# Kernel optimization log

Measured on AMD Instinct MI355X. Metric: run time of the kernel, lower is better.

Reference implementation:

```python
import math
import jax, jax.numpy as jnp
import numpy as np

B, H, S, D = 2, 16, 2048, 1024
DK = D // H  # 64


def setup_inputs() -> dict:
    key = jax.random.key(0)
    k1, k2, k3, k4, k5 = jax.random.split(key, 5)
    scale = np.float32(0.02)
    return {
        "x": jax.random.normal(k1, (B, H, S, D), dtype=jnp.float32),
        "wq": jax.random.normal(k2, (DK, D), dtype=jnp.float32) * scale,
        "wk": jax.random.normal(k3, (DK, D), dtype=jnp.float32) * scale,
        "wv": jax.random.normal(k4, (DK, D), dtype=jnp.float32) * scale,
        "wo": jax.random.normal(k5, (D, D), dtype=jnp.float32) * scale,
    }


def reference(x, wq, wk, wv, wo):
    # x: [B, H, S, D]; wq/wk/wv: [dk, D]; wo: [D, D]
    b, h, s, d = x.shape
    xq = jnp.einsum("bhsd,kd->bhsk", x, wq)  # [B,H,S,dk]
    xk = jnp.einsum("bhsd,kd->bhsk", x, wk)
    xv = jnp.einsum("bhsd,kd->bhsk", x, wv)
    # NOTE: original scales by sqrt(hidden_dim), not sqrt(dk)
    inv_scale = np.float32(1.0 / math.sqrt(d))
    score = jnp.einsum("bhsk,bhtk->bhst", xq, xk) * inv_scale  # [B,H,S,S]
    attn = jax.nn.softmax(score, axis=-1).astype(xq.dtype)
    out = jnp.einsum("bhst,bhtk->bhsk", attn, xv)  # [B,H,S,dk]
    out = out.transpose(0, 2, 1, 3).reshape(b, s, h * (wq.shape[0]))  # [B,S,H*dk]
    return out @ wo.T  # [B,S,D]
```

## Files before the change

### kernel.cpp

```cpp
#include <hip/hip_runtime.h>
#include <math.h>

#define BB 2
#define HH 16
#define SS 2048
#define DD 1024
#define DK 64
#define BHS (BB*HH*SS)
#define QSCALE 0.04508422f

typedef short  bf16x8  __attribute__((ext_vector_type(8)));
typedef float  floatx4 __attribute__((ext_vector_type(4)));
typedef unsigned short u16;

#define MFMA(a,b,c) __builtin_amdgcn_mfma_f32_16x16x32_bf16((a),(b),(c),0,0,0)

__device__ __forceinline__ unsigned cvt_pk_bf16(float lo, float hi) {
    unsigned r;
    asm("v_cvt_pk_bf16_f32 %0, %1, %2" : "=v"(r) : "v"(lo), "v"(hi));
    return r;
}
__device__ __forceinline__ bf16x8 ldfrag(const u16* p) {
    union { uint4 u; bf16x8 b; } c;
    c.u = *(const uint4*)p;
    return c.b;
}
__device__ __forceinline__ void stbf4(u16* p, float4 t) {
    union { unsigned u[2]; uint2 v; } c;
    c.u[0] = cvt_pk_bf16(t.x, t.y);
    c.u[1] = cvt_pk_bf16(t.z, t.w);
    *(uint2*)p = c.v;
}
__device__ __forceinline__ void st4s(u16* p, float a, float b, float c, float d) {
    unsigned x = cvt_pk_bf16(a, b), y = cvt_pk_bf16(c, d);
    p[0]  = (u16)x; p[16] = (u16)(x >> 16);
    p[32] = (u16)y; p[48] = (u16)(y >> 16);
}
__device__ __forceinline__ void st2s(u16* p, float a, float b) {
    unsigned x = cvt_pk_bf16(a, b);
    p[0]  = (u16)x; p[16] = (u16)(x >> 16);
}

#define WQKV_CHUNKS (192*1024/4)
#define WO_CHUNKS   (1024*1024/4)
__global__ __launch_bounds__(256) void convert_w(
    const float* __restrict__ wq, const float* __restrict__ wk,
    const float* __restrict__ wv, const float* __restrict__ wo,
    u16* __restrict__ wqkv, u16* __restrict__ wo_bf)
{
    int i = blockIdx.x * 256 + threadIdx.x;
    if (i < WQKV_CHUNKS) {
        int r = i >> 8;
        int c = i & 255;
        const float* src = (r < 64) ? wq : ((r < 128) ? wk : wv);
        float4 t = *(const float4*)(src + (size_t)(r & 63) * DD + c * 4);
        stbf4(wqkv + (size_t)r * DD + c * 4, t);
    } else if (i < WQKV_CHUNKS + WO_CHUNKS) {
        int j = i - WQKV_CHUNKS;
        float4 t = *(const float4*)(wo + (size_t)j * 4);
        stbf4(wo_bf + (size_t)j * 4, t);
    }
}

__global__ __launch_bounds__(512) void qkv_proj(
    const float* __restrict__ x, const u16* __restrict__ wqkv,
    u16* __restrict__ q, u16* __restrict__ k, u16* __restrict__ vT)
{
    __shared__ __align__(16) u16 Ws[2][192][72];
    const int tid  = threadIdx.x;
    const int w    = tid >> 6;
    const int lane = tid & 63;
    const int quad = lane >> 4;
    const int l16  = lane & 15;
    const int rt   = w & 3;
    const int g    = w >> 2;
    const int rowbase = blockIdx.x * 64;
    const float* xr = x + (size_t)(rowbase + rt * 16 + l16) * DD + quad * 8;

    uint4 wreg[3];
    auto wload = [&](int kk) {
#pragma unroll
        for (int it = 0; it < 3; ++it) {
            int li = tid + it * 512;
            int r  = li >> 3, c8 = li & 7;
            wreg[it] = *(const uint4*)(wqkv + (size_t)r * DD + kk * 64 + c8 * 8);
        }
    };
    auto wstore = [&](int p) {
#pragma unroll
        for (int it = 0; it < 3; ++it) {
            int li = tid + it * 512;
            int r  = li >> 3, c8 = li & 7;
            *(uint4*)&Ws[p][r][c8 * 8] = wreg[it];
        }
    };

    float4 xc[4], xn[4];
    auto xload = [&](int kk, float4* d) {
        const float* p = xr + kk * 64;
        d[0] = *(const float4*)(p);
        d[1] = *(const float4*)(p + 4);
        d[2] = *(const float4*)(p + 32);
        d[3] = *(const float4*)(p + 36);
    };

    floatx4 acc[6];
#pragma unroll
    for (int j = 0; j < 6; ++j) acc[j] = (floatx4){0.f,0.f,0.f,0.f};

    wload(0); wstore(0);
    xload(0, xc);
    __syncthreads();

    for (int kk = 0; kk < 16; ++kk) {
        int p = kk & 1;
        if (kk < 15) { wload(kk + 1); xload(kk + 1, xn); }
        union { unsigned u[4]; bf16x8 v; } A0, A1;
        A0.u[0] = cvt_pk_bf16(xc[0].x, xc[0].y);
        A0.u[1] = cvt_pk_bf16(xc[0].z, xc[0].w);
        A0.u[2] = cvt_pk_bf16(xc[1].x, xc[1].y);
        A0.u[3] = cvt_pk_bf16(xc[1].z, xc[1].w);
        A1.u[0] = cvt_pk_bf16(xc[2].x, xc[2].y);
        A1.u[1] = cvt_pk_bf16(xc[2].z, xc[2].w);
        A1.u[2] = cvt_pk_bf16(xc[3].x, xc[3].y);
        A1.u[3] = cvt_pk_bf16(xc[3].z, xc[3].w);
#pragma unroll
        for (int j = 0; j < 6; ++j) {
            int n = g * 6 + j;
            bf16x8 b0 = ldfrag(&Ws[p][n * 16 + l16][quad * 8]);
            bf16x8 b1 = ldfrag(&Ws[p][n * 16 + l16][32 + quad * 8]);
            acc[j] = MFMA(A0.v, b0, acc[j]);
            acc[j] = MFMA(A1.v, b1, acc[j]);
        }
        if (kk < 15) {
            wstore(p ^ 1);
#pragma unroll
            for (int i2 = 0; i2 < 4; ++i2) xc[i2] = xn[i2];
            __syncthreads();
        }
    }

    u16 (*Vbuf)[72] = (u16 (*)[72])&Ws[0][0][0];
#pragma unroll
    for (int rr = 0; rr < 4; ++rr) {
        int rloc = rt * 16 + quad * 4 + rr;
        size_t m = (size_t)(rowbase + rloc);
        if (g == 0) {
            st4s(&q[m * DK + l16], acc[0][rr] * QSCALE, acc[1][rr] * QSCALE,
                                   acc[2][rr] * QSCALE, acc[3][rr] * QSCALE);
            st2s(&k[m * DK + l16], acc[4][rr], acc[5][rr]);
        } else {
            st2s(&k[m * DK + 32 + l16], acc[0][rr], acc[1][rr]);
            st4s(&Vbuf[rloc][l16], acc[2][rr], acc[3][rr],
                                   acc[4][rr], acc[5][rr]);
        }
    }
    __syncthreads();
    {
        const int dk = tid >> 3;
        const int sc = (tid & 7) * 8;
        const int bh = rowbase >> 11;
        const int s0 = rowbase & 2047;
        union { u16 s[8]; uint4 u; } t;
#pragma unroll
        for (int u = 0; u < 8; ++u) t.s[u] = Vbuf[sc + u][dk];
        *(uint4*)(vT + ((size_t)(bh * DK + dk)) * SS + s0 + sc) = t.u;
    }
}

__global__ __launch_bounds__(256) void flash_attn(
    const u16* __restrict__ q, const u16* __restrict__ k,
    const u16* __restrict__ vT, u16* __restrict__ ao)
{
    __shared__ __align__(16) u16 Qs[64][72];
    __shared__ __align__(16) u16 Ks[64][72];
    __shared__ __align__(16) u16 Vt[64][72];
    __shared__ __align__(16) u16 Ps[4][16][72];
    const int tid  = threadIdx.x;
    const int w    = tid >> 6;
    const int lane = tid & 63;
    const int quad = lane >> 4;
    const int l16  = lane & 15;
    const int qt   = blockIdx.x;
    const int bh   = blockIdx.y;
    const size_t kbase = (size_t)bh * SS * DK;
    const size_t vbase = (size_t)bh * DK * SS;

#pragma unroll
    for (int it = 0; it < 2; ++it) {
        int li = tid + it * 256;
        int r  = li >> 3, c8 = li & 7;
        *(uint4*)&Qs[r][c8 * 8] =
            *(const uint4*)(q + kbase + (size_t)(qt * 64 + r) * DK + c8 * 8);
    }

    float m_i[4], l_i[4];
    floatx4 acc_o[4];
#pragma unroll
    for (int r = 0; r < 4; ++r) { m_i[r] = -INFINITY; l_i[r] = 0.f; }
#pragma unroll
    for (int n = 0; n < 4; ++n) acc_o[n] = (floatx4){0.f,0.f,0.f,0.f};
    __syncthreads();

    for (int kt = 0; kt < SS / 64; ++kt) {
#pragma unroll
        for (int it = 0; it < 2; ++it) {
            int li = tid + it * 256;
            int r  = li >> 3, c8 = li & 7;
            *(uint4*)&Ks[r][c8 * 8] =
                *(const uint4*)(k + kbase + (size_t)(kt * 64 + r) * DK + c8 * 8);
            *(uint4*)&Vt[r][c8 * 8] =
                *(const uint4*)(vT + vbase + (size_t)r * SS + kt * 64 + c8 * 8);
        }
        __syncthreads();

        floatx4 sc[4];
        __builtin_amdgcn_s_setprio(1);
        {
            bf16x8 a0 = ldfrag(&Qs[w * 16 + l16][quad * 8]);
            bf16x8 a1 = ldfrag(&Qs[w * 16 + l16][32 + quad * 8]);
#pragma unroll
            for (int n = 0; n < 4; ++n) {
                sc[n] = (floatx4){0.f,0.f,0.f,0.f};
                bf16x8 b0 = ldfrag(&Ks[n * 16 + l16][quad * 8]);
                bf16x8 b1 = ldfrag(&Ks[n * 16 + l16][32 + quad * 8]);
                sc[n] = MFMA(a0, b0, sc[n]);
                sc[n] = MFMA(a1, b1, sc[n]);
            }
        }
        __builtin_amdgcn_s_setprio(0);

        float rmx[4];
#pragma unroll
        for (int r = 0; r < 4; ++r) {
            float rm = fmaxf(fmaxf(sc[0][r], sc[1][r]), fmaxf(sc[2][r], sc[3][r]));
#pragma unroll
            for (int off = 1; off < 16; off <<= 1)
                rm = fmaxf(rm, __shfl_xor(rm, off, 64));
            rmx[r] = rm;
        }
        int ok = (rmx[0] <= m_i[0] + 8.f) & (rmx[1] <= m_i[1] + 8.f) &
                 (rmx[2] <= m_i[2] + 8.f) & (rmx[3] <= m_i[3] + 8.f);
        if (!__all(ok)) {
#pragma unroll
            for (int r = 0; r < 4; ++r) {
                float mnew  = fmaxf(m_i[r], rmx[r]);
                float alpha = __builtin_amdgcn_exp2f(m_i[r] - mnew);
#pragma unroll
                for (int n = 0; n < 4; ++n) acc_o[n][r] *= alpha;
                l_i[r] *= alpha;
                m_i[r]  = mnew;
            }
        }
#pragma unroll
        for (int r = 0; r < 4; ++r) {
            float mi = m_i[r];
            float p0 = __builtin_amdgcn_exp2f(sc[0][r] - mi);
            float p1 = __builtin_amdgcn_exp2f(sc[1][r] - mi);
            float p2 = __builtin_amdgcn_exp2f(sc[2][r] - mi);
            float p3 = __builtin_amdgcn_exp2f(sc[3][r] - mi);
            float rs = (p0 + p1) + (p2 + p3);
#pragma unroll
            for (int off = 1; off < 16; off <<= 1)
                rs += __shfl_xor(rs, off, 64);
            l_i[r] += rs;
            st4s(&Ps[w][quad * 4 + r][l16], p0, p1, p2, p3);
        }

        __builtin_amdgcn_s_setprio(1);
#pragma unroll
        for (int kc = 0; kc < 2; ++kc) {
            bf16x8 a = ldfrag(&Ps[w][l16][kc * 32 + quad * 8]);
#pragma unroll
            for (int n = 0; n < 4; ++n) {
                bf16x8 b = ldfrag(&Vt[n * 16 + l16][kc * 32 + quad * 8]);
                acc_o[n] = MFMA(a, b, acc_o[n]);
            }
        }
        __builtin_amdgcn_s_setprio(0);
        __syncthreads();
    }

    const int b = bh >> 4, h = bh & 15;
#pragma unroll
    for (int r = 0; r < 4; ++r) {
        int srow = qt * 64 + w * 16 + quad * 4 + r;
        float rl = __builtin_amdgcn_rcpf(l_i[r]);
        size_t base = ((size_t)(b * SS + srow)) * (HH * DK) + h * 64;
        st4s(&ao[base + l16], acc_o[0][r] * rl, acc_o[1][r] * rl,
                              acc_o[2][r] * rl, acc_o[3][r] * rl);
    }
}

__global__ __launch_bounds__(256) void out_proj(
    const u16* __restrict__ ao, const u16* __restrict__ wo_bf,
    float* __restrict__ out)
{
    __shared__ __align__(16) u16 As[64][72];
    __shared__ __align__(16) u16 Bs[64][72];
    const int tid  = threadIdx.x;
    const int w    = tid >> 6;
    const int lane = tid & 63;
    const int quad = lane >> 4;
    const int l16  = lane & 15;
    const int mt = blockIdx.y;
    const int nt = blockIdx.x;

    floatx4 acc[4];
#pragma unroll
    for (int n = 0; n < 4; ++n) acc[n] = (floatx4){0.f,0.f,0.f,0.f};

    for (int k0 = 0; k0 < DD; k0 += 64) {
#pragma unroll
        for (int it = 0; it < 2; ++it) {
            int li = tid + it * 256;
            int r  = li >> 3, c8 = li & 7;
            *(uint4*)&As[r][c8 * 8] =
                *(const uint4*)(ao + (size_t)(mt * 64 + r) * DD + k0 + c8 * 8);
            *(uint4*)&Bs[r][c8 * 8] =
                *(const uint4*)(wo_bf + (size_t)(nt * 64 + r) * DD + k0 + c8 * 8);
        }
        __syncthreads();

        bf16x8 a0 = ldfrag(&As[w * 16 + l16][quad * 8]);
        bf16x8 a1 = ldfrag(&As[w * 16 + l16][32 + quad * 8]);
#pragma unroll
        for (int n = 0; n < 4; ++n) {
            bf16x8 b0 = ldfrag(&Bs[n * 16 + l16][quad * 8]);
            bf16x8 b1 = ldfrag(&Bs[n * 16 + l16][32 + quad * 8]);
            acc[n] = MFMA(a0, b0, acc[n]);
            acc[n] = MFMA(a1, b1, acc[n]);
        }
        __syncthreads();
    }

#pragma unroll
    for (int r = 0; r < 4; ++r) {
        int row = mt * 64 + w * 16 + quad * 4 + r;
#pragma unroll
        for (int n = 0; n < 4; ++n)
            out[(size_t)row * DD + nt * 64 + n * 16 + l16] = acc[n][r];
    }
}

extern "C" void kernel_launch(void* const* d_in, const int* in_sizes, int n_in,
                              void* d_out, int out_size, void* d_ws, size_t ws_size,
                              hipStream_t stream) {
    const float* x  = (const float*)d_in[0];
    const float* wq = (const float*)d_in[1];
    const float* wk = (const float*)d_in[2];
    const float* wv = (const float*)d_in[3];
    const float* wo = (const float*)d_in[4];
    float* out = (float*)d_out;

    u16* q     = (u16*)d_ws;
    u16* k     = q    + (size_t)BHS * DK;
    u16* vT    = k    + (size_t)BHS * DK;
    u16* ao    = vT   + (size_t)BHS * DK;
    u16* wqkv  = ao   + (size_t)BHS * DK;
    u16* wo_bf = wqkv + (size_t)192 * DD;

    convert_w<<<dim3((WQKV_CHUNKS + WO_CHUNKS) / 256), dim3(256), 0, stream>>>(
        wq, wk, wv, wo, wqkv, wo_bf);
    qkv_proj<<<dim3(BHS / 64), dim3(512), 0, stream>>>(x, wqkv, q, k, vT);
    flash_attn<<<dim3(SS / 64, BB * HH), dim3(256), 0, stream>>>(q, k, vT, ao);
    out_proj<<<dim3(DD / 64, (BB * SS) / 64), dim3(256), 0, stream>>>(ao, wo_bf, out);
}
```

Before: 566.6 us.

## Prefetch K/V and GEMM tiles through registers, widen attention and out-proj tiles

Flash attention now keeps the Q fragments in registers rather than LDS, processes 128-key tiles instead of 64, and prefetches the next K/V tile into registers while computing the current one, storing it to LDS after a barrier. The output projection doubles its M tile to 128 rows per block with two accumulator sets, and uses the same register prefetch scheme. The intent is to hide global-memory latency behind MFMA work and halve the number of loop iterations and barriers. In exchange, register pressure rises from prefetch buffers and the larger accumulators, which may lower occupancy, and the out_proj grid halves.

```diff
diff --git a/kernel.cpp b/kernel.cpp
--- a/kernel.cpp
+++ b/kernel.cpp
@@ -172,10 +172,9 @@
     const u16* __restrict__ q, const u16* __restrict__ k,
     const u16* __restrict__ vT, u16* __restrict__ ao)
 {
-    __shared__ __align__(16) u16 Qs[64][72];
-    __shared__ __align__(16) u16 Ks[64][72];
-    __shared__ __align__(16) u16 Vt[64][72];
-    __shared__ __align__(16) u16 Ps[4][16][72];
+    __shared__ __align__(16) u16 Ks[128][72];
+    __shared__ __align__(16) u16 Vt[64][136];
+    __shared__ __align__(16) u16 Ps[4][16][136];
     const int tid  = threadIdx.x;
     const int w    = tid >> 6;
     const int lane = tid & 63;
@@ -186,13 +185,29 @@
     const size_t kbase = (size_t)bh * SS * DK;
     const size_t vbase = (size_t)bh * DK * SS;
 
-#pragma unroll
-    for (int it = 0; it < 2; ++it) {
-        int li = tid + it * 256;
-        int r  = li >> 3, c8 = li & 7;
-        *(uint4*)&Qs[r][c8 * 8] =
-            *(const uint4*)(q + kbase + (size_t)(qt * 64 + r) * DK + c8 * 8);
-    }
+    const u16* qrow = q + kbase + (size_t)(qt * 64 + w * 16 + l16) * DK;
+    const bf16x8 qa0 = ldfrag(qrow + quad * 8);
+    const bf16x8 qa1 = ldfrag(qrow + 32 + quad * 8);
+
+    uint4 kreg[4], vreg[4];
+    auto kvload = [&](int kt) {
+#pragma unroll
+        for (int it = 0; it < 4; ++it) {
+            int li = tid + it * 256;
+            kreg[it] = *(const uint4*)(k + kbase +
+                        (size_t)(kt * 128 + (li >> 3)) * DK + (li & 7) * 8);
+            vreg[it] = *(const uint4*)(vT + vbase +
+                        (size_t)(li >> 4) * SS + kt * 128 + (li & 15) * 8);
+        }
+    };
+    auto kvstore = [&]() {
+#pragma unroll
+        for (int it = 0; it < 4; ++it) {
+            int li = tid + it * 256;
+            *(uint4*)&Ks[li >> 3][(li & 7) * 8]  = kreg[it];
+            *(uint4*)&Vt[li >> 4][(li & 15) * 8] = vreg[it];
+        }
+    };
 
     float m_i[4], l_i[4];
     floatx4 acc_o[4];
@@ -200,40 +215,30 @@
     for (int r = 0; r < 4; ++r) { m_i[r] = -INFINITY; l_i[r] = 0.f; }
 #pragma unroll
     for (int n = 0; n < 4; ++n) acc_o[n] = (floatx4){0.f,0.f,0.f,0.f};
+
+    kvload(0); kvstore();
     __syncthreads();
 
-    for (int kt = 0; kt < SS / 64; ++kt) {
-#pragma unroll
-        for (int it = 0; it < 2; ++it) {
-            int li = tid + it * 256;
-            int r  = li >> 3, c8 = li & 7;
-            *(uint4*)&Ks[r][c8 * 8] =
-                *(const uint4*)(k + kbase + (size_t)(kt * 64 + r) * DK + c8 * 8);
-            *(uint4*)&Vt[r][c8 * 8] =
-                *(const uint4*)(vT + vbase + (size_t)r * SS + kt * 64 + c8 * 8);
-        }
-        __syncthreads();
-
-        floatx4 sc[4];
+    for (int kt = 0; kt < SS / 128; ++kt) {
+        if (kt < SS / 128 - 1) kvload(kt + 1);
+
+        floatx4 sc[8];
         __builtin_amdgcn_s_setprio(1);
-        {
-            bf16x8 a0 = ldfrag(&Qs[w * 16 + l16][quad * 8]);
-            bf16x8 a1 = ldfrag(&Qs[w * 16 + l16][32 + quad * 8]);
-#pragma unroll
-            for (int n = 0; n < 4; ++n) {
-                sc[n] = (floatx4){0.f,0.f,0.f,0.f};
-                bf16x8 b0 = ldfrag(&Ks[n * 16 + l16][quad * 8]);
-                bf16x8 b1 = ldfrag(&Ks[n * 16 + l16][32 + quad * 8]);
-                sc[n] = MFMA(a0, b0, sc[n]);
-                sc[n] = MFMA(a1, b1, sc[n]);
-            }
+#pragma unroll
+        for (int n = 0; n < 8; ++n) {
+            sc[n] = (floatx4){0.f,0.f,0.f,0.f};
+            bf16x8 b0 = ldfrag(&Ks[n * 16 + l16][quad * 8]);
+            bf16x8 b1 = ldfrag(&Ks[n * 16 + l16][32 + quad * 8]);
+            sc[n] = MFMA(qa0, b0, sc[n]);
+            sc[n] = MFMA(qa1, b1, sc[n]);
         }
         __builtin_amdgcn_s_setprio(0);
 
         float rmx[4];
 #pragma unroll
         for (int r = 0; r < 4; ++r) {
-            float rm = fmaxf(fmaxf(sc[0][r], sc[1][r]), fmaxf(sc[2][r], sc[3][r]));
+            float rm = fmaxf(fmaxf(fmaxf(sc[0][r], sc[1][r]), fmaxf(sc[2][r], sc[3][r])),
+                             fmaxf(fmaxf(sc[4][r], sc[5][r]), fmaxf(sc[6][r], sc[7][r])));
 #pragma unroll
             for (int off = 1; off < 16; off <<= 1)
                 rm = fmaxf(rm, __shfl_xor(rm, off, 64));
@@ -259,17 +264,22 @@
             float p1 = __builtin_amdgcn_exp2f(sc[1][r] - mi);
             float p2 = __builtin_amdgcn_exp2f(sc[2][r] - mi);
             float p3 = __builtin_amdgcn_exp2f(sc[3][r] - mi);
-            float rs = (p0 + p1) + (p2 + p3);
+            float p4 = __builtin_amdgcn_exp2f(sc[4][r] - mi);
+            float p5 = __builtin_amdgcn_exp2f(sc[5][r] - mi);
+            float p6 = __builtin_amdgcn_exp2f(sc[6][r] - mi);
+            float p7 = __builtin_amdgcn_exp2f(sc[7][r] - mi);
+            float rs = ((p0 + p1) + (p2 + p3)) + ((p4 + p5) + (p6 + p7));
 #pragma unroll
             for (int off = 1; off < 16; off <<= 1)
                 rs += __shfl_xor(rs, off, 64);
             l_i[r] += rs;
-            st4s(&Ps[w][quad * 4 + r][l16], p0, p1, p2, p3);
+            st4s(&Ps[w][quad * 4 + r][l16],      p0, p1, p2, p3);
+            st4s(&Ps[w][quad * 4 + r][64 + l16], p4, p5, p6, p7);
         }
 
         __builtin_amdgcn_s_setprio(1);
 #pragma unroll
-        for (int kc = 0; kc < 2; ++kc) {
+        for (int kc = 0; kc < 4; ++kc) {
             bf16x8 a = ldfrag(&Ps[w][l16][kc * 32 + quad * 8]);
 #pragma unroll
             for (int n = 0; n < 4; ++n) {
@@ -278,6 +288,8 @@
             }
         }
         __builtin_amdgcn_s_setprio(0);
+        __syncthreads();
+        if (kt < SS / 128 - 1) kvstore();
         __syncthreads();
     }
 
@@ -296,7 +308,7 @@
     const u16* __restrict__ ao, const u16* __restrict__ wo_bf,
     float* __restrict__ out)
 {
-    __shared__ __align__(16) u16 As[64][72];
+    __shared__ __align__(16) u16 As[128][72];
     __shared__ __align__(16) u16 Bs[64][72];
     const int tid  = threadIdx.x;
     const int w    = tid >> 6;
@@ -306,40 +318,70 @@
     const int mt = blockIdx.y;
     const int nt = blockIdx.x;
 
-    floatx4 acc[4];
-#pragma unroll
-    for (int n = 0; n < 4; ++n) acc[n] = (floatx4){0.f,0.f,0.f,0.f};
-
-    for (int k0 = 0; k0 < DD; k0 += 64) {
+    uint4 areg[4], breg[2];
+    auto abload = [&](int kk) {
+#pragma unroll
+        for (int it = 0; it < 4; ++it) {
+            int li = tid + it * 256;
+            areg[it] = *(const uint4*)(ao + (size_t)(mt * 128 + (li >> 3)) * DD
+                                          + kk * 64 + (li & 7) * 8);
+        }
 #pragma unroll
         for (int it = 0; it < 2; ++it) {
             int li = tid + it * 256;
-            int r  = li >> 3, c8 = li & 7;
-            *(uint4*)&As[r][c8 * 8] =
-                *(const uint4*)(ao + (size_t)(mt * 64 + r) * DD + k0 + c8 * 8);
-            *(uint4*)&Bs[r][c8 * 8] =
-                *(const uint4*)(wo_bf + (size_t)(nt * 64 + r) * DD + k0 + c8 * 8);
+            breg[it] = *(const uint4*)(wo_bf + (size_t)(nt * 64 + (li >> 3)) * DD
+                                             + kk * 64 + (li & 7) * 8);
+        }
+    };
+    auto abstore = [&]() {
+#pragma unroll
+        for (int it = 0; it < 4; ++it) {
+            int li = tid + it * 256;
+            *(uint4*)&As[li >> 3][(li & 7) * 8] = areg[it];
+        }
+#pragma unroll
+        for (int it = 0; it < 2; ++it) {
+            int li = tid + it * 256;
+            *(uint4*)&Bs[li >> 3][(li & 7) * 8] = breg[it];
+        }
+    };
+
+    floatx4 acc[2][4];
+#pragma unroll
+    for (int rt = 0; rt < 2; ++rt)
+#pragma unroll
+        for (int n = 0; n < 4; ++n) acc[rt][n] = (floatx4){0.f,0.f,0.f,0.f};
+
+    abload(0); abstore();
+    __syncthreads();
+
+    for (int kk = 0; kk < 16; ++kk) {
+        if (kk < 15) abload(kk + 1);
+#pragma unroll
+        for (int kc = 0; kc < 2; ++kc) {
+            bf16x8 a0 = ldfrag(&As[w * 32 + l16][kc * 32 + quad * 8]);
+            bf16x8 a1 = ldfrag(&As[w * 32 + 16 + l16][kc * 32 + quad * 8]);
+#pragma unroll
+            for (int n = 0; n < 4; ++n) {
+                bf16x8 b = ldfrag(&Bs[n * 16 + l16][kc * 32 + quad * 8]);
+                acc[0][n] = MFMA(a0, b, acc[0][n]);
+                acc[1][n] = MFMA(a1, b, acc[1][n]);
+            }
         }
         __syncthreads();
-
-        bf16x8 a0 = ldfrag(&As[w * 16 + l16][quad * 8]);
-        bf16x8 a1 = ldfrag(&As[w * 16 + l16][32 + quad * 8]);
-#pragma unroll
-        for (int n = 0; n < 4; ++n) {
-            bf16x8 b0 = ldfrag(&Bs[n * 16 + l16][quad * 8]);
-            bf16x8 b1 = ldfrag(&Bs[n * 16 + l16][32 + quad * 8]);
-            acc[n] = MFMA(a0, b0, acc[n]);
-            acc[n] = MFMA(a1, b1, acc[n]);
-        }
+        if (kk < 15) abstore();
         __syncthreads();
     }
 
 #pragma unroll
-    for (int r = 0; r < 4; ++r) {
-        int row = mt * 64 + w * 16 + quad * 4 + r;
-#pragma unroll
-        for (int n = 0; n < 4; ++n)
-            out[(size_t)row * DD + nt * 64 + n * 16 + l16] = acc[n][r];
+    for (int rt = 0; rt < 2; ++rt) {
+#pragma unroll
+        for (int rr = 0; rr < 4; ++rr) {
+            int row = mt * 128 + w * 32 + rt * 16 + quad * 4 + rr;
+#pragma unroll
+            for (int n = 0; n < 4; ++n)
+                out[(size_t)row * DD + nt * 64 + n * 16 + l16] = acc[rt][n][rr];
+        }
     }
 }
 
@@ -364,5 +406,5 @@
         wq, wk, wv, wo, wqkv, wo_bf);
     qkv_proj<<<dim3(BHS / 64), dim3(512), 0, stream>>>(x, wqkv, q, k, vT);
     flash_attn<<<dim3(SS / 64, BB * HH), dim3(256), 0, stream>>>(q, k, vT, ao);
-    out_proj<<<dim3(DD / 64, (BB * SS) / 64), dim3(256), 0, stream>>>(ao, wo_bf, out);
-}
+    out_proj<<<dim3(DD / 64, (BB * SS) / 128), dim3(256), 0, stream>>>(ao, wo_bf, out);
+}
```

Result: slower. 634.5 us (+12.0%).

## Widen attention KV tile, keep Q in registers, defer reductions, enlarge out_proj tile

Applied to the files above, without the earlier changes.

flash_attn now processes 128 keys per iteration with Q fragments held in registers instead of LDS. It defers the cross-lane row-sum shuffle to the epilogue and only shuffles the row max when a rescale is needed. The block index is remapped so that neighbouring blocks share heads for L2 locality. out_proj moves to 128x128 tiles with 512 threads to cut global traffic per FLOP. The new LDS row strides (68 and 132 elements) are not 16-byte multiples, so 128-bit LDS fragment loads may be misaligned, and register pressure rises from eight score accumulators.

```diff
diff --git a/kernel.cpp b/kernel.cpp
--- a/kernel.cpp
+++ b/kernel.cpp
@@ -172,84 +172,80 @@
     const u16* __restrict__ q, const u16* __restrict__ k,
     const u16* __restrict__ vT, u16* __restrict__ ao)
 {
-    __shared__ __align__(16) u16 Qs[64][72];
-    __shared__ __align__(16) u16 Ks[64][72];
-    __shared__ __align__(16) u16 Vt[64][72];
-    __shared__ __align__(16) u16 Ps[4][16][72];
+    __shared__ __align__(16) u16 Ks[128][68];
+    __shared__ __align__(16) u16 Vt[64][132];
+    __shared__ __align__(16) u16 Ps[4][16][132];
     const int tid  = threadIdx.x;
     const int w    = tid >> 6;
     const int lane = tid & 63;
     const int quad = lane >> 4;
     const int l16  = lane & 15;
-    const int qt   = blockIdx.x;
-    const int bh   = blockIdx.y;
+    const int L  = blockIdx.y * 32 + blockIdx.x;
+    const int qt = (L >> 3) & 31;
+    const int bh = (L & 7) * 4 + (L >> 8);
     const size_t kbase = (size_t)bh * SS * DK;
     const size_t vbase = (size_t)bh * DK * SS;
 
-#pragma unroll
-    for (int it = 0; it < 2; ++it) {
-        int li = tid + it * 256;
-        int r  = li >> 3, c8 = li & 7;
-        *(uint4*)&Qs[r][c8 * 8] =
-            *(const uint4*)(q + kbase + (size_t)(qt * 64 + r) * DK + c8 * 8);
-    }
-
-    float m_i[4], l_i[4];
+    const u16* qrow = q + kbase + (size_t)(qt * 64 + w * 16 + l16) * DK;
+    const bf16x8 qa0 = ldfrag(qrow + quad * 8);
+    const bf16x8 qa1 = ldfrag(qrow + 32 + quad * 8);
+
+    float m_i[4], l_part[4];
     floatx4 acc_o[4];
 #pragma unroll
-    for (int r = 0; r < 4; ++r) { m_i[r] = -INFINITY; l_i[r] = 0.f; }
+    for (int r = 0; r < 4; ++r) { m_i[r] = -INFINITY; l_part[r] = 0.f; }
 #pragma unroll
     for (int n = 0; n < 4; ++n) acc_o[n] = (floatx4){0.f,0.f,0.f,0.f};
-    __syncthreads();
-
-    for (int kt = 0; kt < SS / 64; ++kt) {
-#pragma unroll
-        for (int it = 0; it < 2; ++it) {
+
+    for (int kt = 0; kt < SS / 128; ++kt) {
+#pragma unroll
+        for (int it = 0; it < 4; ++it) {
             int li = tid + it * 256;
-            int r  = li >> 3, c8 = li & 7;
-            *(uint4*)&Ks[r][c8 * 8] =
-                *(const uint4*)(k + kbase + (size_t)(kt * 64 + r) * DK + c8 * 8);
-            *(uint4*)&Vt[r][c8 * 8] =
-                *(const uint4*)(vT + vbase + (size_t)r * SS + kt * 64 + c8 * 8);
+            *(uint4*)&Ks[li >> 3][(li & 7) * 8] =
+                *(const uint4*)(k + kbase + (size_t)(kt * 128 + (li >> 3)) * DK
+                                + (li & 7) * 8);
+        }
+#pragma unroll
+        for (int it = 0; it < 4; ++it) {
+            int li = tid + it * 256;
+            *(uint4*)&Vt[li >> 4][(li & 15) * 8] =
+                *(const uint4*)(vT + vbase + (size_t)(li >> 4) * SS
+                                + kt * 128 + (li & 15) * 8);
         }
         __syncthreads();
 
-        floatx4 sc[4];
+        floatx4 sc[8];
         __builtin_amdgcn_s_setprio(1);
-        {
-            bf16x8 a0 = ldfrag(&Qs[w * 16 + l16][quad * 8]);
-            bf16x8 a1 = ldfrag(&Qs[w * 16 + l16][32 + quad * 8]);
-#pragma unroll
-            for (int n = 0; n < 4; ++n) {
-                sc[n] = (floatx4){0.f,0.f,0.f,0.f};
-                bf16x8 b0 = ldfrag(&Ks[n * 16 + l16][quad * 8]);
-                bf16x8 b1 = ldfrag(&Ks[n * 16 + l16][32 + quad * 8]);
-                sc[n] = MFMA(a0, b0, sc[n]);
-                sc[n] = MFMA(a1, b1, sc[n]);
-            }
+#pragma unroll
+        for (int n = 0; n < 8; ++n) {
+            sc[n] = (floatx4){0.f,0.f,0.f,0.f};
+            bf16x8 b0 = ldfrag(&Ks[n * 16 + l16][quad * 8]);
+            bf16x8 b1 = ldfrag(&Ks[n * 16 + l16][32 + quad * 8]);
+            sc[n] = MFMA(qa0, b0, sc[n]);
+            sc[n] = MFMA(qa1, b1, sc[n]);
         }
         __builtin_amdgcn_s_setprio(0);
 
-        float rmx[4];
-#pragma unroll
-        for (int r = 0; r < 4; ++r) {
-            float rm = fmaxf(fmaxf(sc[0][r], sc[1][r]), fmaxf(sc[2][r], sc[3][r]));
-#pragma unroll
-            for (int off = 1; off < 16; off <<= 1)
-                rm = fmaxf(rm, __shfl_xor(rm, off, 64));
-            rmx[r] = rm;
-        }
-        int ok = (rmx[0] <= m_i[0] + 8.f) & (rmx[1] <= m_i[1] + 8.f) &
-                 (rmx[2] <= m_i[2] + 8.f) & (rmx[3] <= m_i[3] + 8.f);
+        float lm[4];
+#pragma unroll
+        for (int r = 0; r < 4; ++r)
+            lm[r] = fmaxf(fmaxf(fmaxf(sc[0][r], sc[1][r]), fmaxf(sc[2][r], sc[3][r])),
+                          fmaxf(fmaxf(sc[4][r], sc[5][r]), fmaxf(sc[6][r], sc[7][r])));
+        int ok = (lm[0] <= m_i[0] + 8.f) & (lm[1] <= m_i[1] + 8.f) &
+                 (lm[2] <= m_i[2] + 8.f) & (lm[3] <= m_i[3] + 8.f);
         if (!__all(ok)) {
 #pragma unroll
             for (int r = 0; r < 4; ++r) {
-                float mnew  = fmaxf(m_i[r], rmx[r]);
+                float rm = lm[r];
+#pragma unroll
+                for (int off = 1; off < 16; off <<= 1)
+                    rm = fmaxf(rm, __shfl_xor(rm, off, 64));
+                float mnew  = fmaxf(m_i[r], rm);
                 float alpha = __builtin_amdgcn_exp2f(m_i[r] - mnew);
 #pragma unroll
                 for (int n = 0; n < 4; ++n) acc_o[n][r] *= alpha;
-                l_i[r] *= alpha;
-                m_i[r]  = mnew;
+                l_part[r] *= alpha;
+                m_i[r]     = mnew;
             }
         }
 #pragma unroll
@@ -259,17 +255,18 @@
             float p1 = __builtin_amdgcn_exp2f(sc[1][r] - mi);
             float p2 = __builtin_amdgcn_exp2f(sc[2][r] - mi);
             float p3 = __builtin_amdgcn_exp2f(sc[3][r] - mi);
-            float rs = (p0 + p1) + (p2 + p3);
-#pragma unroll
-            for (int off = 1; off < 16; off <<= 1)
-                rs += __shfl_xor(rs, off, 64);
-            l_i[r] += rs;
-            st4s(&Ps[w][quad * 4 + r][l16], p0, p1, p2, p3);
+            float p4 = __builtin_amdgcn_exp2f(sc[4][r] - mi);
+            float p5 = __builtin_amdgcn_exp2f(sc[5][r] - mi);
+            float p6 = __builtin_amdgcn_exp2f(sc[6][r] - mi);
+            float p7 = __builtin_amdgcn_exp2f(sc[7][r] - mi);
+            l_part[r] += ((p0 + p1) + (p2 + p3)) + ((p4 + p5) + (p6 + p7));
+            st4s(&Ps[w][quad * 4 + r][l16],      p0, p1, p2, p3);
+            st4s(&Ps[w][quad * 4 + r][64 + l16], p4, p5, p6, p7);
         }
 
         __builtin_amdgcn_s_setprio(1);
 #pragma unroll
-        for (int kc = 0; kc < 2; ++kc) {
+        for (int kc = 0; kc < 4; ++kc) {
             bf16x8 a = ldfrag(&Ps[w][l16][kc * 32 + quad * 8]);
 #pragma unroll
             for (int n = 0; n < 4; ++n) {
@@ -284,20 +281,24 @@
     const int b = bh >> 4, h = bh & 15;
 #pragma unroll
     for (int r = 0; r < 4; ++r) {
+        float l = l_part[r];
+#pragma unroll
+        for (int off = 1; off < 16; off <<= 1)
+            l += __shfl_xor(l, off, 64);
+        float rl = __builtin_amdgcn_rcpf(l);
         int srow = qt * 64 + w * 16 + quad * 4 + r;
-        float rl = __builtin_amdgcn_rcpf(l_i[r]);
         size_t base = ((size_t)(b * SS + srow)) * (HH * DK) + h * 64;
         st4s(&ao[base + l16], acc_o[0][r] * rl, acc_o[1][r] * rl,
                               acc_o[2][r] * rl, acc_o[3][r] * rl);
     }
 }
 
-__global__ __launch_bounds__(256) void out_proj(
+__global__ __launch_bounds__(512) void out_proj(
     const u16* __restrict__ ao, const u16* __restrict__ wo_bf,
     float* __restrict__ out)
 {
-    __shared__ __align__(16) u16 As[64][72];
-    __shared__ __align__(16) u16 Bs[64][72];
+    __shared__ __align__(16) u16 As[128][68];
+    __shared__ __align__(16) u16 Bs[128][68];
     const int tid  = threadIdx.x;
     const int w    = tid >> 6;
     const int lane = tid & 63;
@@ -306,26 +307,26 @@
     const int mt = blockIdx.y;
     const int nt = blockIdx.x;
 
-    floatx4 acc[4];
-#pragma unroll
-    for (int n = 0; n < 4; ++n) acc[n] = (floatx4){0.f,0.f,0.f,0.f};
-
-    for (int k0 = 0; k0 < DD; k0 += 64) {
+    floatx4 acc[8];
+#pragma unroll
+    for (int n = 0; n < 8; ++n) acc[n] = (floatx4){0.f,0.f,0.f,0.f};
+
+    for (int kk = 0; kk < 16; ++kk) {
 #pragma unroll
         for (int it = 0; it < 2; ++it) {
-            int li = tid + it * 256;
+            int li = tid + it * 512;
             int r  = li >> 3, c8 = li & 7;
             *(uint4*)&As[r][c8 * 8] =
-                *(const uint4*)(ao + (size_t)(mt * 64 + r) * DD + k0 + c8 * 8);
+                *(const uint4*)(ao + (size_t)(mt * 128 + r) * DD + kk * 64 + c8 * 8);
             *(uint4*)&Bs[r][c8 * 8] =
-                *(const uint4*)(wo_bf + (size_t)(nt * 64 + r) * DD + k0 + c8 * 8);
+                *(const uint4*)(wo_bf + (size_t)(nt * 128 + r) * DD + kk * 64 + c8 * 8);
         }
         __syncthreads();
 
         bf16x8 a0 = ldfrag(&As[w * 16 + l16][quad * 8]);
         bf16x8 a1 = ldfrag(&As[w * 16 + l16][32 + quad * 8]);
 #pragma unroll
-        for (int n = 0; n < 4; ++n) {
+        for (int n = 0; n < 8; ++n) {
             bf16x8 b0 = ldfrag(&Bs[n * 16 + l16][quad * 8]);
             bf16x8 b1 = ldfrag(&Bs[n * 16 + l16][32 + quad * 8]);
             acc[n] = MFMA(a0, b0, acc[n]);
@@ -335,11 +336,11 @@
     }
 
 #pragma unroll
-    for (int r = 0; r < 4; ++r) {
-        int row = mt * 64 + w * 16 + quad * 4 + r;
-#pragma unroll
-        for (int n = 0; n < 4; ++n)
-            out[(size_t)row * DD + nt * 64 + n * 16 + l16] = acc[n][r];
+    for (int rr = 0; rr < 4; ++rr) {
+        int row = mt * 128 + w * 16 + quad * 4 + rr;
+#pragma unroll
+        for (int n = 0; n < 8; ++n)
+            out[(size_t)row * DD + nt * 128 + n * 16 + l16] = acc[n][rr];
     }
 }
 
@@ -363,6 +364,6 @@
     convert_w<<<dim3((WQKV_CHUNKS + WO_CHUNKS) / 256), dim3(256), 0, stream>>>(
         wq, wk, wv, wo, wqkv, wo_bf);
     qkv_proj<<<dim3(BHS / 64), dim3(512), 0, stream>>>(x, wqkv, q, k, vT);
-    flash_attn<<<dim3(SS / 64, BB * HH), dim3(256), 0, stream>>>(q, k, vT, ao);
-    out_proj<<<dim3(DD / 64, (BB * SS) / 64), dim3(256), 0, stream>>>(ao, wo_bf, out);
-}
+    flash_attn<<<dim3(32, 32), dim3(256), 0, stream>>>(q, k, vT, ao);
+    out_proj<<<dim3(DD / 128, (BB * SS) / 128), dim3(512), 0, stream>>>(ao, wo_bf, out);
+}
```

After: 784.4 us. 38.4% more time.
